# Kernel tuning notes

Hardware: AMD Instinct MI355X
Metric: run time of the kernel (lower is better)

## Reference

```python
import jax, jax.numpy as jnp
import numpy as np

NMS_PRE, NMS_POST, NMS_THRESH = 1024, 512, 0.7
B, A, FEAT = 4, 70400, 27648
BN_EPS = 1e-5


def _bev_iou(boxes):
    # boxes: [K, 7] (x, y, z, dx, dy, dz, ry); axis-aligned BEV IoU
    x, y, dx, dy = boxes[:, 0], boxes[:, 1], boxes[:, 3], boxes[:, 4]
    x1, x2 = x - 0.5 * dx, x + 0.5 * dx
    y1, y2 = y - 0.5 * dy, y + 0.5 * dy
    iw = jnp.clip(jnp.minimum(x2[:, None], x2[None, :]) - jnp.maximum(x1[:, None], x1[None, :]), 0.0)
    ih = jnp.clip(jnp.minimum(y2[:, None], y2[None, :]) - jnp.maximum(y1[:, None], y1[None, :]), 0.0)
    inter = iw * ih
    area = dx * dy
    return inter / jnp.clip(area[:, None] + area[None, :] - inter, 1e-6)


def _greedy_nms(boxes, thresh):
    # boxes sorted by score desc; returns keep mask [K]
    K = boxes.shape[0]
    iou = _bev_iou(boxes)
    idx = jnp.arange(K)

    def step(keep, i):
        sup = (iou[i] > thresh) & (idx > i) & keep[i]
        return keep & ~sup, None

    keep, _ = jax.lax.scan(step, jnp.ones(K, dtype=bool), jnp.arange(K))
    return keep


def _proposal_one(box, cls):
    # box: [A, 7], cls: [A, n_cls]  ->  padded rois [NPOST,7], scores [NPOST], labels [NPOST]
    score = jnp.max(cls, axis=-1)
    label = jnp.argmax(cls, axis=-1)
    top_score, top_idx = jax.lax.top_k(score, NMS_PRE)
    top_box = box[top_idx]
    keep = _greedy_nms(top_box, NMS_THRESH)
    # stable: kept entries first, preserving score order
    order = jnp.argsort(jnp.where(keep, jnp.arange(NMS_PRE), NMS_PRE + jnp.arange(NMS_PRE)))
    sel = order[:NMS_POST]
    valid = jnp.arange(NMS_POST) < jnp.minimum(jnp.sum(keep), NMS_POST)
    rois = jnp.where(valid[:, None], top_box[sel], 0.0)
    roi_score = jnp.where(valid, top_score[sel], 0.0)
    roi_label = jnp.where(valid, label[top_idx][sel], 0) + 1  # +1 as in module
    return rois, roi_score, roi_label


def _bn_relu(h, g, b):
    # eval-mode BN with running_mean=0, running_var=1
    return jax.nn.relu(h * (g / jnp.sqrt(1.0 + BN_EPS)) + b)


def _decode(reg, anchors):
    # ResidualCoder_v1.decode_torch
    xa, ya, za = anchors[..., 0], anchors[..., 1], anchors[..., 2]
    dxa, dya, dza, ra = anchors[..., 3], anchors[..., 4], anchors[..., 5], anchors[..., 6]
    xt, yt, zt = reg[..., 0], reg[..., 1], reg[..., 2]
    dxt, dyt, dzt, rt = reg[..., 3], reg[..., 4], reg[..., 5], reg[..., 6]
    diag = jnp.sqrt(dxa * dxa + dya * dya)
    return jnp.stack([
        xt * diag + xa, yt * diag + ya, zt * dza + za,
        jnp.exp(dxt) * dxa, jnp.exp(dyt) * dya, jnp.exp(dzt) * dza,
        rt + ra], axis=-1)


def _rotate_z(box, ang):
    # rotate x,y of box [..., 7] by ang [...]
    c, s = jnp.cos(ang), jnp.sin(ang)
    x = box[..., 0] * c - box[..., 1] * s
    y = box[..., 0] * s + box[..., 1] * c
    return jnp.concatenate([x[..., None], y[..., None], box[..., 2:]], axis=-1)


def reference(rpn_box_preds, rpn_cls_preds, pooled_features,
              Ws1, g1, b1, Ws2, g2, b2,
              Wc1, gc1, bc1, Wc2, gc2, bc2, Wc3, bc3,
              Wr1, gr1, br1, Wr2, gr2, br2, Wr3, br3):
    # proposal_layer: per-batch topk + NMS + padded scatter (vmapped)
    rois, roi_scores, roi_labels = jax.vmap(_proposal_one)(rpn_box_preds, rpn_cls_preds)

    # shared / cls / reg heads (1x1 Conv1d == per-roi MLP), dropout off (eval)
    x = _bn_relu(pooled_features @ Ws1.T, g1, b1)
    x = _bn_relu(x @ Ws2.T, g2, b2)
    c = _bn_relu(x @ Wc1.T, gc1, bc1)
    c = _bn_relu(c @ Wc2.T, gc2, bc2)
    cls_preds = c @ Wc3.T + bc3          # [B*NPOST, 1]
    r = _bn_relu(x @ Wr1.T, gr1, br1)
    r = _bn_relu(r @ Wr2.T, gr2, br2)
    reg_preds = r @ Wr3.T + br3          # [B*NPOST, 7]

    bsz = rois.shape[0]
    cls_preds = cls_preds.reshape(bsz, -1, cls_preds.shape[-1])
    reg_preds = reg_preds.reshape(bsz, -1, 7)

    # generate_predict_box: decode against detached rois with xyz zeroed
    anchors = jax.lax.stop_gradient(rois)
    anchors = anchors.at[..., 0:3].set(0.0)
    box_ct = _decode(reg_preds, anchors)
    box_preds = _rotate_z(box_ct, rois[..., 6])
    box_preds = jnp.concatenate([box_preds[..., 0:3] + rois[..., 0:3], box_preds[..., 3:]], axis=-1)

    return jnp.concatenate([cls_preds, box_preds, roi_scores[..., None]], axis=-1)  # [B, NPOST, 9]


def setup_inputs():
    key = jax.random.key(0)
    ks = jax.random.split(key, 32)
    u = jax.random.uniform(ks[0], (B, A, 7), dtype=jnp.float32)
    lo = jnp.array([0.0, -40.0, -2.0, 1.5, 1.4, 1.0, -3.14159], jnp.float32)
    hi = jnp.array([70.0, 40.0, 0.0, 4.5, 2.0, 2.0, 3.14159], jnp.float32)
    rpn_box_preds = lo + u * (hi - lo)
    rpn_cls_preds = jax.random.normal(ks[1], (B, A, 3), dtype=jnp.float32)
    pooled_features = jax.random.normal(ks[2], (B * NMS_POST, FEAT), dtype=jnp.float32) * 0.1

    def w(k, o, i, std=None):
        s = (1.0 / np.sqrt(i)) if std is None else std
        return jax.random.normal(k, (o, i), dtype=jnp.float32) * s

    d = dict(
        rpn_box_preds=rpn_box_preds, rpn_cls_preds=rpn_cls_preds, pooled_features=pooled_features,
        Ws1=w(ks[3], 256, FEAT), g1=jnp.ones(256), b1=jnp.zeros(256),
        Ws2=w(ks[4], 256, 256), g2=jnp.ones(256), b2=jnp.zeros(256),
        Wc1=w(ks[5], 256, 256), gc1=jnp.ones(256), bc1=jnp.zeros(256),
        Wc2=w(ks[6], 256, 256), gc2=jnp.ones(256), bc2=jnp.zeros(256),
        Wc3=w(ks[7], 1, 256), bc3=jnp.zeros(1),
        Wr1=w(ks[8], 256, 256), gr1=jnp.ones(256), br1=jnp.zeros(256),
        Wr2=w(ks[9], 256, 256), gr2=jnp.ones(256), br2=jnp.zeros(256),
        Wr3=w(ks[10], 7, 256, std=0.001), br3=jnp.zeros(7),
    )
    return d
```

## Files before the change

### kernel.cpp

```cpp
#include <hip/hip_runtime.h>
#include <cstdint>

typedef unsigned int u32;
typedef unsigned long long u64;
typedef unsigned short u16;

#define BATCH 4
#define A_CNT 70400
#define FEAT 27648
#define KSPLIT 16
#define KCHUNK 1728
#define NTILE_IT 27

typedef __attribute__((ext_vector_type(8))) short bf16x8;
typedef __attribute__((ext_vector_type(4))) float f32x4;
typedef __attribute__((ext_vector_type(4))) u32 u32x4;

constexpr size_t OF_KEYS = 0;
constexpr size_t OF_TBOX = OF_KEYS + 1126400;
constexpr size_t OF_TSC  = OF_TBOX + 114688;
constexpr size_t OF_BX1  = OF_TSC + 16384;
constexpr size_t OF_BX2  = OF_BX1 + 16384;
constexpr size_t OF_BY1  = OF_BX2 + 16384;
constexpr size_t OF_BY2  = OF_BY1 + 16384;
constexpr size_t OF_BAR  = OF_BY2 + 16384;
constexpr size_t OF_MASK = OF_BAR + 16384;
constexpr size_t OF_ROIS = OF_MASK + 524288;
constexpr size_t OF_RSC  = OF_ROIS + 57344;
constexpr size_t OF_BSW  = OF_RSC + 8192;
constexpr size_t OF_PART = OF_BSW + 14155776;
constexpr size_t WS_NEED = OF_PART + 33554432;

__device__ __forceinline__ u32 keyOf(float f) {
  u32 u = __float_as_uint(f);
  return (u & 0x80000000u) ? ~u : (u | 0x80000000u);
}
__device__ __forceinline__ float keyToF(u32 k) {
  u32 u = (k & 0x80000000u) ? (k ^ 0x80000000u) : ~k;
  return __uint_as_float(u);
}
__device__ __forceinline__ u16 f2bf(float f) {
  u32 u = __float_as_uint(f);
  u32 r = 0x7FFFu + ((u >> 16) & 1u);
  return (u16)((u + r) >> 16);
}
__device__ __forceinline__ void gload_lds16(const void* g, void* l) {
  auto gp = reinterpret_cast<const __attribute__((address_space(1))) unsigned int*>(
      reinterpret_cast<uintptr_t>(g));
  auto lp = reinterpret_cast<__attribute__((address_space(3))) unsigned int*>(
      reinterpret_cast<uintptr_t>(l));
  __builtin_amdgcn_global_load_lds(gp, lp, 16, 0, 0);
}
__device__ __forceinline__ u64 shflx64(u64 v, int m) {
  u32 lo = (u32)v, hi = (u32)(v >> 32);
  lo = __shfl_xor(lo, m, 64);
  hi = __shfl_xor(hi, m, 64);
  return ((u64)hi << 32) | lo;
}

__global__ __launch_bounds__(1024) void k_fatA(const float* __restrict__ cls,
    const float* __restrict__ Ws1, u32* __restrict__ keys, u32* __restrict__ Bsw)
{
  int bid = blockIdx.x;
  int t = threadIdx.x;
  if (bid < 864) {
    u32 w = (u32)bid * 1024u + t;
    u32 tile = w >> 11;
    u32 rem = w & 2047u;
    u32 n = rem >> 3;
    u32 pq = (rem & 7u) << 4;
    u32 q0 = pq ^ ((n & 7u) << 4);
    u32 col0 = tile * 64u + (q0 >> 1);
    const float* src = Ws1 + (size_t)n * FEAT + col0;
    float4 f0 = *(const float4*)src;
    float4 f1 = *(const float4*)(src + 4);
    u32x4 o;
    o.x = (u32)f2bf(f0.x) | ((u32)f2bf(f0.y) << 16);
    o.y = (u32)f2bf(f0.z) | ((u32)f2bf(f0.w) << 16);
    o.z = (u32)f2bf(f1.x) | ((u32)f2bf(f1.y) << 16);
    o.w = (u32)f2bf(f1.z) | ((u32)f2bf(f1.w) << 16);
    ((u32x4*)Bsw)[w] = o;
    return;
  }
  u32 g = (u32)(bid - 864) * 1024u + t;
  float s0 = cls[(size_t)g * 3 + 0];
  float s1 = cls[(size_t)g * 3 + 1];
  float s2 = cls[(size_t)g * 3 + 2];
  keys[g] = keyOf(fmaxf(s0, fmaxf(s1, s2)));
}

__global__ __launch_bounds__(1024) void k_prop(const u32* __restrict__ keys,
    const float* __restrict__ boxes, float* __restrict__ tbox, float* __restrict__ tsc,
    float* __restrict__ bx1, float* __restrict__ bx2, float* __restrict__ by1,
    float* __restrict__ by2, float* __restrict__ bar)
{
  int b = blockIdx.x, t = threadIdx.x;
  int lane = t & 63, wv = t >> 6;
  const u32* kb = keys + (size_t)b * A_CNT;
  __shared__ u64 s[2048];
  __shared__ u32 partials[16];
  __shared__ u32 cc;
  u32 h[35];
#pragma unroll
  for (int j = 0; j < 35; ++j) {
    int g0 = t + ((2 * j) << 10);
    int g1 = t + ((2 * j + 1) << 10);
    u32 a = (g0 < A_CNT) ? (kb[g0] >> 16) : 0u;
    u32 c2 = (g1 < A_CNT) ? (kb[g1] >> 16) : 0u;
    h[j] = a | (c2 << 16);
  }
  if (t == 0) cc = 0u;
  u32 lo = 0, hi = 65536;
  while (hi - lo > 1) {
    u32 mid = (lo + hi) >> 1;
    u32 c = 0;
#pragma unroll
    for (int j = 0; j < 35; ++j) {
      c += ((h[j] & 0xFFFFu) >= mid) ? 1u : 0u;
      c += ((h[j] >> 16) >= mid) ? 1u : 0u;
    }
#pragma unroll
    for (int o = 32; o > 0; o >>= 1) c += __shfl_xor(c, o, 64);
    __syncthreads();
    if (lane == 0) partials[wv] = c;
    __syncthreads();
    u32 tot = 0;
#pragma unroll
    for (int w2 = 0; w2 < 16; ++w2) tot += partials[w2];
    if (tot >= 1024u) lo = mid; else hi = mid;
  }
  u32 kth = lo;
  __syncthreads();
  u32 kc = kb[t];
#pragma unroll 1
  for (int i = 0; i < 69; ++i) {
    int g = t + (i << 10);
    u32 k = kc;
    if (i < 68) {
      int gn = t + ((i + 1) << 10);
      kc = (gn < A_CNT) ? kb[gn] : 0u;
    }
    bool pass = (g < A_CNT) && ((k >> 16) >= kth);
    u64 mm = __ballot(pass);
    if (mm) {
      int leader = __ffsll((unsigned long long)mm) - 1;
      u32 base = 0;
      if (lane == leader) base = atomicAdd(&cc, (u32)__popcll(mm));
      base = __shfl(base, leader, 64);
      if (pass) {
        u32 pos = base + (u32)__popcll(mm & ((1ull << lane) - 1ull));
        if (pos < 2048u) s[pos] = ((u64)k << 32) | (u32)(~(u32)g);
      }
    }
  }
  __syncthreads();
  u32 m = cc; if (m > 2048u) m = 2048u;
  for (int e = t; e < 2048; e += 1024) if (e >= (int)m) s[e] = 0ull;
  __syncthreads();
  {
    u64 v0 = s[2 * t], v1 = s[2 * t + 1];
#pragma unroll
    for (u32 k = 2; k <= 128; k <<= 1) {
      bool desc = ((t & (k >> 1)) == 0);
#pragma unroll
      for (u32 j = (k >> 1); j >= 2; j >>= 1) {
        u32 mmk = j >> 1;
        u64 p0 = shflx64(v0, mmk);
        u64 p1 = shflx64(v1, mmk);
        bool up = ((t & mmk) == 0);
        bool mx = (desc == up);
        v0 = mx ? (v0 > p0 ? v0 : p0) : (v0 < p0 ? v0 : p0);
        v1 = mx ? (v1 > p1 ? v1 : p1) : (v1 < p1 ? v1 : p1);
      }
      if (desc ? (v0 < v1) : (v0 > v1)) { u64 tmp = v0; v0 = v1; v1 = tmp; }
    }
    s[2 * t] = v0; s[2 * t + 1] = v1;
    __syncthreads();
    for (u32 k = 256; k <= 2048; k <<= 1) {
      for (u32 j = k >> 1; j >= 128; j >>= 1) {
        for (int e = t; e < 2048; e += 1024) {
          u32 p = (u32)e ^ j;
          if (p > (u32)e) {
            bool d2 = ((e & k) == 0);
            u64 x = s[e], y = s[p];
            if (d2 ? (x < y) : (x > y)) { s[e] = y; s[p] = x; }
          }
        }
        __syncthreads();
      }
      u64 v0 = s[2 * t], v1 = s[2 * t + 1];
      bool desc = ((t & (k >> 1)) == 0);
#pragma unroll
      for (u32 j = 64; j >= 2; j >>= 1) {
        u32 mmk = j >> 1;
        u64 p0 = shflx64(v0, mmk);
        u64 p1 = shflx64(v1, mmk);
        bool up = ((t & mmk) == 0);
        bool mx = (desc == up);
        v0 = mx ? (v0 > p0 ? v0 : p0) : (v0 < p0 ? v0 : p0);
        v1 = mx ? (v1 > p1 ? v1 : p1) : (v1 < p1 ? v1 : p1);
      }
      if (desc ? (v0 < v1) : (v0 > v1)) { u64 tmp = v0; v0 = v1; v1 = tmp; }
      s[2 * t] = v0; s[2 * t + 1] = v1;
      __syncthreads();
    }
  }
  u64 comp = s[t];
  u32 kk = (u32)(comp >> 32);
  u32 a = ~(u32)(comp & 0xFFFFFFFFull);
  int o = b * 1024 + t;
  tsc[o] = keyToF(kk);
  const float* bp = boxes + ((size_t)b * A_CNT + a) * 7;
  float x = bp[0], y = bp[1], z = bp[2], dx = bp[3], dy = bp[4], dz = bp[5], rr = bp[6];
  float* tb = tbox + (size_t)o * 7;
  tb[0] = x; tb[1] = y; tb[2] = z; tb[3] = dx; tb[4] = dy; tb[5] = dz; tb[6] = rr;
  {
#pragma clang fp contract(off)
    bx1[o] = x - 0.5f * dx; bx2[o] = x + 0.5f * dx;
    by1[o] = y - 0.5f * dy; by2[o] = y + 0.5f * dy;
    bar[o] = dx * dy;
  }
}

__global__ __launch_bounds__(256) void k_fatB(const float* __restrict__ A,
    const u32* __restrict__ Bsw, float* __restrict__ part,
    const float* __restrict__ bx1, const float* __restrict__ bx2,
    const float* __restrict__ by1, const float* __restrict__ by2,
    const float* __restrict__ bar, u32* __restrict__ mask)
{
  __shared__ __align__(16) char smem[73728];
  int bid = blockIdx.x;
  if (bid >= 512) {
    int mi = bid - 512;
    int b = mi >> 6;
    int cbk = (mi >> 2) & 15;
    int rb0 = (mi & 3) * 4;
    int tt = threadIdx.x;
    int rbi = tt >> 6, ln = tt & 63;
    int r = (rb0 + rbi) * 64 + ln;
    int o = b * 1024, jc0 = cbk * 64;
    float* cx1 = (float*)(smem);
    float* cx2 = (float*)(smem + 256);
    float* cy1 = (float*)(smem + 512);
    float* cy2 = (float*)(smem + 768);
    float* car = (float*)(smem + 1024);
    if (tt < 64) {
      cx1[tt] = bx1[o + jc0 + tt]; cx2[tt] = bx2[o + jc0 + tt];
      cy1[tt] = by1[o + jc0 + tt]; cy2[tt] = by2[o + jc0 + tt];
      car[tt] = bar[o + jc0 + tt];
    }
    __syncthreads();
    float rx1 = bx1[o + r], rx2 = bx2[o + r], ry1 = by1[o + r], ry2 = by2[o + r], rar = bar[o + r];
    u32 w0 = 0, w1 = 0;
    {
#pragma clang fp contract(off)
      for (int c = 0; c < 64; ++c) {
        int jc = jc0 + c;
        float iw = fminf(rx2, cx2[c]) - fmaxf(rx1, cx1[c]); iw = fmaxf(iw, 0.0f);
        float ih = fminf(ry2, cy2[c]) - fmaxf(ry1, cy1[c]); ih = fmaxf(ih, 0.0f);
        float inter = iw * ih;
        float den = fmaxf(rar + car[c] - inter, 1e-6f);
        float iou = inter / den;
        if ((iou > 0.7f) && (jc > r)) {
          if (c < 32) w0 |= 1u << c; else w1 |= 1u << (c - 32);
        }
      }
    }
    mask[((size_t)(o + r)) * 32 + cbk * 2 + 0] = w0;
    mask[((size_t)(o + r)) * 32 + cbk * 2 + 1] = w1;
    return;
  }
  int q = bid >> 3;
  int ks = (bid & 7) * 2 + (q >> 5);
  int mt = q & 31;
  int tid = threadIdx.x, lane = tid & 63, wv = tid >> 6;

  f32x4 acc[4][4];
#pragma unroll
  for (int i = 0; i < 4; ++i)
#pragma unroll
    for (int j = 0; j < 4; ++j) acc[i][j] = (f32x4){0.f, 0.f, 0.f, 0.f};

  int am = tid >> 2;
  int ak = (tid & 3) * 16;
  const float* ap_base = A + ((size_t)(mt * 64 + am)) * FEAT + (size_t)ks * KCHUNK + ak;
  int asw = (am & 7) << 4;
  int ac0 = (tid & 3) * 32;
  int awoff0 = am * 128 + (ac0 ^ asw);
  int awoff1 = am * 128 + ((ac0 + 16) ^ asw);
  const char* bsrc_base = (const char*)Bsw + ((size_t)(ks * NTILE_IT)) * 32768 + (wv * 8) * 1024 + lane * 16;
  int bdoff = (wv * 8) * 1024;

  int row16 = lane & 15, kgrp = lane >> 4;
  int aoff[4][2], boff[4][2];
#pragma unroll
  for (int ksub = 0; ksub < 2; ++ksub) {
    int qq = ksub * 64 + kgrp * 16;
#pragma unroll
    for (int mf = 0; mf < 4; ++mf) {
      int row = mf * 16 + row16;
      aoff[mf][ksub] = row * 128 + (qq ^ ((row & 7) << 4));
    }
#pragma unroll
    for (int nf = 0; nf < 4; ++nf) {
      int n = wv * 64 + nf * 16 + row16;
      boff[nf][ksub] = n * 128 + (qq ^ ((n & 7) << 4));
    }
  }

  char* Albuf = smem;
  {
    const float4* ap = (const float4*)ap_base;
    float4 f0 = ap[0], f1 = ap[1], f2 = ap[2], f3 = ap[3];
    u32x4 c0, c1;
    c0.x = (u32)f2bf(f0.x) | ((u32)f2bf(f0.y) << 16);
    c0.y = (u32)f2bf(f0.z) | ((u32)f2bf(f0.w) << 16);
    c0.z = (u32)f2bf(f1.x) | ((u32)f2bf(f1.y) << 16);
    c0.w = (u32)f2bf(f1.z) | ((u32)f2bf(f1.w) << 16);
    c1.x = (u32)f2bf(f2.x) | ((u32)f2bf(f2.y) << 16);
    c1.y = (u32)f2bf(f2.z) | ((u32)f2bf(f2.w) << 16);
    c1.z = (u32)f2bf(f3.x) | ((u32)f2bf(f3.y) << 16);
    c1.w = (u32)f2bf(f3.z) | ((u32)f2bf(f3.w) << 16);
    *(u32x4*)(Albuf + awoff0) = c0;
    *(u32x4*)(Albuf + awoff1) = c1;
#pragma unroll
    for (int i = 0; i < 8; ++i)
      gload_lds16(bsrc_base + i * 1024, smem + 8192 + bdoff + i * 1024);
  }
  __syncthreads();

  for (int it = 0; it < NTILE_IT; ++it) {
    char* Bcur = smem + 8192 + ((it & 1) ? 32768 : 0);
    char* Bnxt = smem + 8192 + ((it & 1) ? 0 : 32768);
    bool has = (it + 1 < NTILE_IT);
    float4 f0n, f1n, f2n, f3n;
    if (has) {
      const float4* ap = (const float4*)(ap_base + (it + 1) * 64);
      f0n = ap[0]; f1n = ap[1]; f2n = ap[2]; f3n = ap[3];
    }
    bf16x8 af[4][2], bfv[4][2];
#pragma unroll
    for (int ksub = 0; ksub < 2; ++ksub) {
#pragma unroll
      for (int mf = 0; mf < 4; ++mf) af[mf][ksub] = *(const bf16x8*)(Albuf + aoff[mf][ksub]);
#pragma unroll
      for (int nf = 0; nf < 4; ++nf) bfv[nf][ksub] = *(const bf16x8*)(Bcur + boff[nf][ksub]);
    }
    __syncthreads();
    if (has) {
      u32x4 c0, c1;
      c0.x = (u32)f2bf(f0n.x) | ((u32)f2bf(f0n.y) << 16);
      c0.y = (u32)f2bf(f0n.z) | ((u32)f2bf(f0n.w) << 16);
      c0.z = (u32)f2bf(f1n.x) | ((u32)f2bf(f1n.y) << 16);
      c0.w = (u32)f2bf(f1n.z) | ((u32)f2bf(f1n.w) << 16);
      c1.x = (u32)f2bf(f2n.x) | ((u32)f2bf(f2n.y) << 16);
      c1.y = (u32)f2bf(f2n.z) | ((u32)f2bf(f2n.w) << 16);
      c1.z = (u32)f2bf(f3n.x) | ((u32)f2bf(f3n.y) << 16);
      c1.w = (u32)f2bf(f3n.z) | ((u32)f2bf(f3n.w) << 16);
      *(u32x4*)(Albuf + awoff0) = c0;
      *(u32x4*)(Albuf + awoff1) = c1;
      const char* bs = bsrc_base + (size_t)(it + 1) * 32768;
#pragma unroll
      for (int i = 0; i < 8; ++i)
        gload_lds16(bs + i * 1024, Bnxt + bdoff + i * 1024);
    }
#pragma unroll
    for (int ksub = 0; ksub < 2; ++ksub)
#pragma unroll
      for (int mf = 0; mf < 4; ++mf)
#pragma unroll
        for (int nf = 0; nf < 4; ++nf)
          acc[mf][nf] = __builtin_amdgcn_mfma_f32_16x16x32_bf16(af[mf][ksub], bfv[nf][ksub], acc[mf][nf], 0, 0, 0);
    __syncthreads();
  }
  float* pb = part + (size_t)ks * 524288;
#pragma unroll
  for (int mf = 0; mf < 4; ++mf) {
    int row = mt * 64 + mf * 16 + kgrp * 4;
#pragma unroll
    for (int nf = 0; nf < 4; ++nf) {
      int col = wv * 64 + nf * 16 + row16;
#pragma unroll
      for (int rr = 0; rr < 4; ++rr)
        pb[(size_t)(row + rr) * 256 + col] = acc[mf][nf][rr];
    }
  }
}

__global__ __launch_bounds__(64) void k_nms(const u32* __restrict__ mask,
    const float* __restrict__ tbox, const float* __restrict__ tsc,
    float* __restrict__ rois, float* __restrict__ rsc)
{
  int b = blockIdx.x;
  int lane = threadIdx.x;
  int el = lane & 31;
  const u32* M = mask + (size_t)b * 1024 * 32;
  u32 R = 0;
  u32 cur[32], nxt[32];
#pragma unroll
  for (int i = 0; i < 32; ++i) cur[i] = M[(size_t)(i * 32 + el)];
#pragma unroll 1
  for (int c = 0; c < 32; ++c) {
    if (c < 31) {
      int nb = (c + 1) * 1024 + el;
#pragma unroll
      for (int i = 0; i < 32; ++i) nxt[i] = M[(size_t)(nb + i * 32)];
    }
    u32 w = R;
#pragma unroll
    for (int i = 0; i < 32; ++i) w |= ((w >> i) & 1u) ? 0u : cur[i];
    u32 wfin = __shfl(w, c, 64);
#pragma unroll
    for (int i = 0; i < 32; ++i) R |= ((wfin >> i) & 1u) ? 0u : cur[i];
#pragma unroll
    for (int i = 0; i < 32; ++i) cur[i] = nxt[i];
  }
  u32 keepw = (lane < 32) ? ~R : 0u;
  int c = __popc(keepw);
  int pre = c;
  for (int d = 1; d < 64; d <<= 1) {
    int v = __shfl_up(pre, d, 64);
    if (lane >= d) pre += v;
  }
  int total = __shfl(pre, 31, 64);
  int base = pre - c;
  if (lane < 32) {
    u32 w = keepw;
    int rank = base;
    while (w) {
      int bit = __ffs(w) - 1;
      w &= w - 1;
      if (rank < 512) {
        int r = lane * 32 + bit;
        const float* tb = tbox + ((size_t)b * 1024 + r) * 7;
        float* rp = rois + ((size_t)b * 512 + rank) * 7;
        rp[0] = tb[0]; rp[1] = tb[1]; rp[2] = tb[2]; rp[3] = tb[3];
        rp[4] = tb[4]; rp[5] = tb[5]; rp[6] = tb[6];
        rsc[b * 512 + rank] = tsc[b * 1024 + r];
      }
      rank++;
    }
  }
  for (int z = total + lane; z < 512; z += 64) {
    float* rp = rois + ((size_t)b * 512 + z) * 7;
    rp[0] = rp[1] = rp[2] = rp[3] = rp[4] = rp[5] = rp[6] = 0.0f;
    rsc[b * 512 + z] = 0.0f;
  }
}

__device__ __forceinline__ void layer4(const float (*IN)[256], const float* __restrict__ W,
    const float* __restrict__ g, const float* __restrict__ bb, float (*OUT)[256], int t, int h)
{
  float acc[4] = {0, 0, 0, 0};
  const float* Wrow = W + (size_t)t * 256;
  for (int k = 0; k < 256; k += 4) {
    float4 w4 = *(const float4*)&Wrow[k];
#pragma unroll
    for (int r = 0; r < 4; ++r) {
      float4 xv = *(const float4*)&IN[h * 4 + r][k];
      acc[r] = fmaf(xv.x, w4.x, acc[r]);
      acc[r] = fmaf(xv.y, w4.y, acc[r]);
      acc[r] = fmaf(xv.z, w4.z, acc[r]);
      acc[r] = fmaf(xv.w, w4.w, acc[r]);
    }
  }
  float sc = g[t] / sqrtf(1.0f + 1e-5f);
  float bv = bb[t];
#pragma unroll
  for (int r = 0; r < 4; ++r)
    OUT[h * 4 + r][t] = fmaxf(fmaf(acc[r], sc, bv), 0.0f);
}

__global__ __launch_bounds__(512) void k_chain(const float* __restrict__ part,
    const float* __restrict__ Ws2, const float* __restrict__ Wc1, const float* __restrict__ Wc2,
    const float* __restrict__ Wr1, const float* __restrict__ Wr2,
    const float* __restrict__ g1, const float* __restrict__ b1,
    const float* __restrict__ g2, const float* __restrict__ b2,
    const float* __restrict__ gc1, const float* __restrict__ bc1,
    const float* __restrict__ gc2, const float* __restrict__ bc2,
    const float* __restrict__ gr1, const float* __restrict__ br1,
    const float* __restrict__ gr2, const float* __restrict__ br2,
    const float* __restrict__ Wc3, const float* __restrict__ bc3,
    const float* __restrict__ Wr3, const float* __restrict__ br3,
    const float* __restrict__ rois, const float* __restrict__ rsc,
    float* __restrict__ out)
{
  int bid = blockIdx.x, tid = threadIdx.x;
  int t = tid & 255, h = tid >> 8;
  __shared__ __align__(16) float bufX[8][256];
  __shared__ __align__(16) float bufY[8][256];
  __shared__ __align__(16) float bufC[8][256];
  __shared__ __align__(16) float bufR[8][256];
  __shared__ float hd[64];
  {
    float sc = g1[t] / sqrtf(1.0f + 1e-5f);
    float bv = b1[t];
#pragma unroll
    for (int r = 0; r < 4; ++r) {
      int row = h * 4 + r;
      float s = 0.f;
#pragma unroll
      for (int ks = 0; ks < KSPLIT; ++ks)
        s += part[(size_t)ks * 524288 + (size_t)(bid * 8 + row) * 256 + t];
      bufX[row][t] = fmaxf(fmaf(s, sc, bv), 0.0f);
    }
  }
  __syncthreads();
  layer4(bufX, Ws2, g2, b2, bufY, t, h);
  __syncthreads();
  layer4(bufY, Wc1, gc1, bc1, bufC, t, h);
  layer4(bufY, Wr1, gr1, br1, bufR, t, h);
  __syncthreads();
  layer4(bufC, Wc2, gc2, bc2, bufX, t, h);
  layer4(bufR, Wr2, gr2, br2, bufY, t, h);
  __syncthreads();
  int wv = tid >> 6, ln = tid & 63;
  for (int task = wv; task < 64; task += 8) {
    float p;
    if (task < 8) {
      float4 yv = *(const float4*)&bufX[task][ln * 4];
      float4 w4 = ((const float4*)Wc3)[ln];
      p = yv.x * w4.x + yv.y * w4.y + yv.z * w4.z + yv.w * w4.w;
    } else {
      int i = task - 8, row = i / 7, j = i % 7;
      float4 yv = *(const float4*)&bufY[row][ln * 4];
      float4 w4 = ((const float4*)(Wr3 + j * 256))[ln];
      p = yv.x * w4.x + yv.y * w4.y + yv.z * w4.z + yv.w * w4.w;
    }
#pragma unroll
    for (int off = 32; off > 0; off >>= 1) p += __shfl_xor(p, off, 64);
    if (ln == 0) hd[task] = p;
  }
  __syncthreads();
  if (tid < 8) {
    int m = bid * 8 + tid;
    float clsv = hd[tid] + bc3[0];
    float rg[7];
#pragma unroll
    for (int j = 0; j < 7; ++j) rg[j] = hd[8 + tid * 7 + j] + br3[j];
    const float* R = rois + (size_t)m * 7;
    float rx = R[0], ry = R[1], rz = R[2], dxa = R[3], dya = R[4], dza = R[5], ra = R[6];
    float diag = sqrtf(dxa * dxa + dya * dya);
    float x = rg[0] * diag, y = rg[1] * diag, z = rg[2] * dza;
    float ex = expf(rg[3]) * dxa, ey = expf(rg[4]) * dya, ez = expf(rg[5]) * dza;
    float hr = rg[6] + ra;
    float cc = cosf(ra), sn = sinf(ra);
    float xr = x * cc - y * sn, yr = x * sn + y * cc;
    float* O = out + (size_t)m * 9;
    O[0] = clsv; O[1] = xr + rx; O[2] = yr + ry; O[3] = z + rz;
    O[4] = ex; O[5] = ey; O[6] = ez; O[7] = hr; O[8] = rsc[m];
  }
}

extern "C" void kernel_launch(void* const* d_in, const int* in_sizes, int n_in,
                              void* d_out, int out_size, void* d_ws, size_t ws_size,
                              hipStream_t stream)
{
  const float* rpn_box = (const float*)d_in[0];
  const float* rpn_cls = (const float*)d_in[1];
  const float* pooled  = (const float*)d_in[2];
  const float* Ws1 = (const float*)d_in[3];
  const float* g1  = (const float*)d_in[4];
  const float* b1  = (const float*)d_in[5];
  const float* Ws2 = (const float*)d_in[6];
  const float* g2  = (const float*)d_in[7];
  const float* b2  = (const float*)d_in[8];
  const float* Wc1 = (const float*)d_in[9];
  const float* gc1 = (const float*)d_in[10];
  const float* bc1 = (const float*)d_in[11];
  const float* Wc2 = (const float*)d_in[12];
  const float* gc2 = (const float*)d_in[13];
  const float* bc2 = (const float*)d_in[14];
  const float* Wc3 = (const float*)d_in[15];
  const float* bc3 = (const float*)d_in[16];
  const float* Wr1 = (const float*)d_in[17];
  const float* gr1 = (const float*)d_in[18];
  const float* br1 = (const float*)d_in[19];
  const float* Wr2 = (const float*)d_in[20];
  const float* gr2 = (const float*)d_in[21];
  const float* br2 = (const float*)d_in[22];
  const float* Wr3 = (const float*)d_in[23];
  const float* br3 = (const float*)d_in[24];

  if (ws_size < WS_NEED) return;

  char* ws = (char*)d_ws;
  u32* keys = (u32*)(ws + OF_KEYS);
  float* tbox = (float*)(ws + OF_TBOX);
  float* tsc  = (float*)(ws + OF_TSC);
  float* bx1 = (float*)(ws + OF_BX1);
  float* bx2 = (float*)(ws + OF_BX2);
  float* by1 = (float*)(ws + OF_BY1);
  float* by2 = (float*)(ws + OF_BY2);
  float* bar = (float*)(ws + OF_BAR);
  u32* mask = (u32*)(ws + OF_MASK);
  float* roisb = (float*)(ws + OF_ROIS);
  float* rscb  = (float*)(ws + OF_RSC);
  u32* Bsw = (u32*)(ws + OF_BSW);
  float* part = (float*)(ws + OF_PART);

  k_fatA<<<1139, 1024, 0, stream>>>(rpn_cls, Ws1, keys, Bsw);
  k_prop<<<4, 1024, 0, stream>>>(keys, rpn_box, tbox, tsc, bx1, bx2, by1, by2, bar);
  k_fatB<<<768, 256, 0, stream>>>(pooled, Bsw, part, bx1, bx2, by1, by2, bar, mask);
  k_nms<<<4, 64, 0, stream>>>(mask, tbox, tsc, roisb, rscb);
  k_chain<<<256, 512, 0, stream>>>(part, Ws2, Wc1, Wc2, Wr1, Wr2,
                                   g1, b1, g2, b2, gc1, bc1, gc2, bc2,
                                   gr1, br1, gr2, br2, Wc3, bc3, Wr3, br3,
                                   roisb, rscb, (float*)d_out);
}
```

Before: 265.8 us.

## Enlarge GEMM M-tile to 128 rows and move double buffering from B to A

The split-K GEMM block now computes a 128x256 output tile instead of 64x256, halving the number of GEMM blocks and the number of times each bf16 weight tile is fetched. The A operand (fp32 converted to bf16) is now double-buffered in LDS, while B is single-buffered and refilled right after its fragments are read into registers. A packing helper replaces the repeated conversion code. The cost is twice as many accumulator registers per thread and only 256 GEMM blocks, which may reduce occupancy and latency hiding on the streaming A loads.

```diff
diff --git a/kernel.cpp b/kernel.cpp
--- a/kernel.cpp
+++ b/kernel.cpp
@@ -56,6 +56,14 @@
   lo = __shfl_xor(lo, m, 64);
   hi = __shfl_xor(hi, m, 64);
   return ((u64)hi << 32) | lo;
+}
+__device__ __forceinline__ u32x4 pack8(float4 a, float4 b) {
+  u32x4 o;
+  o.x = (u32)f2bf(a.x) | ((u32)f2bf(a.y) << 16);
+  o.y = (u32)f2bf(a.z) | ((u32)f2bf(a.w) << 16);
+  o.z = (u32)f2bf(b.x) | ((u32)f2bf(b.y) << 16);
+  o.w = (u32)f2bf(b.z) | ((u32)f2bf(b.w) << 16);
+  return o;
 }
 
 __global__ __launch_bounds__(1024) void k_fatA(const float* __restrict__ cls,
@@ -74,12 +82,7 @@
     const float* src = Ws1 + (size_t)n * FEAT + col0;
     float4 f0 = *(const float4*)src;
     float4 f1 = *(const float4*)(src + 4);
-    u32x4 o;
-    o.x = (u32)f2bf(f0.x) | ((u32)f2bf(f0.y) << 16);
-    o.y = (u32)f2bf(f0.z) | ((u32)f2bf(f0.w) << 16);
-    o.z = (u32)f2bf(f1.x) | ((u32)f2bf(f1.y) << 16);
-    o.w = (u32)f2bf(f1.z) | ((u32)f2bf(f1.w) << 16);
-    ((u32x4*)Bsw)[w] = o;
+    ((u32x4*)Bsw)[w] = pack8(f0, f1);
     return;
   }
   u32 g = (u32)(bid - 864) * 1024u + t;
@@ -228,10 +231,10 @@
     const float* __restrict__ by1, const float* __restrict__ by2,
     const float* __restrict__ bar, u32* __restrict__ mask)
 {
-  __shared__ __align__(16) char smem[73728];
+  __shared__ __align__(16) char smem[65536];
   int bid = blockIdx.x;
-  if (bid >= 512) {
-    int mi = bid - 512;
+  if (bid >= 256) {
+    int mi = bid - 256;
     int b = mi >> 6;
     int cbk = (mi >> 2) & 15;
     int rb0 = (mi & 3) * 4;
@@ -270,34 +273,35 @@
     mask[((size_t)(o + r)) * 32 + cbk * 2 + 1] = w1;
     return;
   }
-  int q = bid >> 3;
-  int ks = (bid & 7) * 2 + (q >> 5);
-  int mt = q & 31;
+  int ks = bid & 15;
+  int mt = bid >> 4;
   int tid = threadIdx.x, lane = tid & 63, wv = tid >> 6;
 
-  f32x4 acc[4][4];
-#pragma unroll
-  for (int i = 0; i < 4; ++i)
+  f32x4 acc[8][4];
+#pragma unroll
+  for (int i = 0; i < 8; ++i)
 #pragma unroll
     for (int j = 0; j < 4; ++j) acc[i][j] = (f32x4){0.f, 0.f, 0.f, 0.f};
 
-  int am = tid >> 2;
-  int ak = (tid & 3) * 16;
-  const float* ap_base = A + ((size_t)(mt * 64 + am)) * FEAT + (size_t)ks * KCHUNK + ak;
+  int am = tid >> 1;
+  int ak = (tid & 1) * 32;
+  const float* ap_base = A + ((size_t)(mt * 128 + am)) * FEAT + (size_t)ks * KCHUNK + ak;
   int asw = (am & 7) << 4;
-  int ac0 = (tid & 3) * 32;
-  int awoff0 = am * 128 + (ac0 ^ asw);
-  int awoff1 = am * 128 + ((ac0 + 16) ^ asw);
+  int aw0 = am * 128 + (((tid & 1) * 64 +  0) ^ asw);
+  int aw1 = am * 128 + (((tid & 1) * 64 + 16) ^ asw);
+  int aw2 = am * 128 + (((tid & 1) * 64 + 32) ^ asw);
+  int aw3 = am * 128 + (((tid & 1) * 64 + 48) ^ asw);
   const char* bsrc_base = (const char*)Bsw + ((size_t)(ks * NTILE_IT)) * 32768 + (wv * 8) * 1024 + lane * 16;
   int bdoff = (wv * 8) * 1024;
+  char* Bbuf = smem + 32768;
 
   int row16 = lane & 15, kgrp = lane >> 4;
-  int aoff[4][2], boff[4][2];
+  int aoff[8][2], boff[4][2];
 #pragma unroll
   for (int ksub = 0; ksub < 2; ++ksub) {
     int qq = ksub * 64 + kgrp * 16;
 #pragma unroll
-    for (int mf = 0; mf < 4; ++mf) {
+    for (int mf = 0; mf < 8; ++mf) {
       int row = mf * 16 + row16;
       aoff[mf][ksub] = row * 128 + (qq ^ ((row & 7) << 4));
     }
@@ -308,75 +312,64 @@
     }
   }
 
-  char* Albuf = smem;
   {
     const float4* ap = (const float4*)ap_base;
-    float4 f0 = ap[0], f1 = ap[1], f2 = ap[2], f3 = ap[3];
-    u32x4 c0, c1;
-    c0.x = (u32)f2bf(f0.x) | ((u32)f2bf(f0.y) << 16);
-    c0.y = (u32)f2bf(f0.z) | ((u32)f2bf(f0.w) << 16);
-    c0.z = (u32)f2bf(f1.x) | ((u32)f2bf(f1.y) << 16);
-    c0.w = (u32)f2bf(f1.z) | ((u32)f2bf(f1.w) << 16);
-    c1.x = (u32)f2bf(f2.x) | ((u32)f2bf(f2.y) << 16);
-    c1.y = (u32)f2bf(f2.z) | ((u32)f2bf(f2.w) << 16);
-    c1.z = (u32)f2bf(f3.x) | ((u32)f2bf(f3.y) << 16);
-    c1.w = (u32)f2bf(f3.z) | ((u32)f2bf(f3.w) << 16);
-    *(u32x4*)(Albuf + awoff0) = c0;
-    *(u32x4*)(Albuf + awoff1) = c1;
+    float4 g0 = ap[0], g1 = ap[1], g2 = ap[2], g3 = ap[3];
+    float4 g4 = ap[4], g5 = ap[5], g6 = ap[6], g7 = ap[7];
+    *(u32x4*)(smem + aw0) = pack8(g0, g1);
+    *(u32x4*)(smem + aw1) = pack8(g2, g3);
+    *(u32x4*)(smem + aw2) = pack8(g4, g5);
+    *(u32x4*)(smem + aw3) = pack8(g6, g7);
 #pragma unroll
     for (int i = 0; i < 8; ++i)
-      gload_lds16(bsrc_base + i * 1024, smem + 8192 + bdoff + i * 1024);
+      gload_lds16(bsrc_base + i * 1024, Bbuf + bdoff + i * 1024);
   }
   __syncthreads();
 
   for (int it = 0; it < NTILE_IT; ++it) {
-    char* Bcur = smem + 8192 + ((it & 1) ? 32768 : 0);
-    char* Bnxt = smem + 8192 + ((it & 1) ? 0 : 32768);
+    char* Acur = smem + ((it & 1) ? 16384 : 0);
+    char* Anxt = smem + ((it & 1) ? 0 : 16384);
     bool has = (it + 1 < NTILE_IT);
-    float4 f0n, f1n, f2n, f3n;
+    float4 g0, g1, g2, g3, g4, g5, g6, g7;
     if (has) {
       const float4* ap = (const float4*)(ap_base + (it + 1) * 64);
-      f0n = ap[0]; f1n = ap[1]; f2n = ap[2]; f3n = ap[3];
-    }
-    bf16x8 af[4][2], bfv[4][2];
-#pragma unroll
-    for (int ksub = 0; ksub < 2; ++ksub) {
-#pragma unroll
-      for (int mf = 0; mf < 4; ++mf) af[mf][ksub] = *(const bf16x8*)(Albuf + aoff[mf][ksub]);
-#pragma unroll
-      for (int nf = 0; nf < 4; ++nf) bfv[nf][ksub] = *(const bf16x8*)(Bcur + boff[nf][ksub]);
-    }
+      g0 = ap[0]; g1 = ap[1]; g2 = ap[2]; g3 = ap[3];
+      g4 = ap[4]; g5 = ap[5]; g6 = ap[6]; g7 = ap[7];
+    }
+    bf16x8 bfv[4][2];
+#pragma unroll
+    for (int ksub = 0; ksub < 2; ++ksub)
+#pragma unroll
+      for (int nf = 0; nf < 4; ++nf)
+        bfv[nf][ksub] = *(const bf16x8*)(Bbuf + boff[nf][ksub]);
     __syncthreads();
     if (has) {
-      u32x4 c0, c1;
-      c0.x = (u32)f2bf(f0n.x) | ((u32)f2bf(f0n.y) << 16);
-      c0.y = (u32)f2bf(f0n.z) | ((u32)f2bf(f0n.w) << 16);
-      c0.z = (u32)f2bf(f1n.x) | ((u32)f2bf(f1n.y) << 16);
-      c0.w = (u32)f2bf(f1n.z) | ((u32)f2bf(f1n.w) << 16);
-      c1.x = (u32)f2bf(f2n.x) | ((u32)f2bf(f2n.y) << 16);
-      c1.y = (u32)f2bf(f2n.z) | ((u32)f2bf(f2n.w) << 16);
-      c1.z = (u32)f2bf(f3n.x) | ((u32)f2bf(f3n.y) << 16);
-      c1.w = (u32)f2bf(f3n.z) | ((u32)f2bf(f3n.w) << 16);
-      *(u32x4*)(Albuf + awoff0) = c0;
-      *(u32x4*)(Albuf + awoff1) = c1;
       const char* bs = bsrc_base + (size_t)(it + 1) * 32768;
 #pragma unroll
       for (int i = 0; i < 8; ++i)
-        gload_lds16(bs + i * 1024, Bnxt + bdoff + i * 1024);
+        gload_lds16(bs + i * 1024, Bbuf + bdoff + i * 1024);
     }
 #pragma unroll
     for (int ksub = 0; ksub < 2; ++ksub)
 #pragma unroll
-      for (int mf = 0; mf < 4; ++mf)
+      for (int mf = 0; mf < 8; ++mf) {
+        bf16x8 af = *(const bf16x8*)(Acur + aoff[mf][ksub]);
 #pragma unroll
         for (int nf = 0; nf < 4; ++nf)
-          acc[mf][nf] = __builtin_amdgcn_mfma_f32_16x16x32_bf16(af[mf][ksub], bfv[nf][ksub], acc[mf][nf], 0, 0, 0);
+          acc[mf][nf] = __builtin_amdgcn_mfma_f32_16x16x32_bf16(af, bfv[nf][ksub], acc[mf][nf], 0, 0, 0);
+      }
+    if (has) {
+      *(u32x4*)(Anxt + aw0) = pack8(g0, g1);
+      *(u32x4*)(Anxt + aw1) = pack8(g2, g3);
+      *(u32x4*)(Anxt + aw2) = pack8(g4, g5);
+      *(u32x4*)(Anxt + aw3) = pack8(g6, g7);
+    }
     __syncthreads();
   }
   float* pb = part + (size_t)ks * 524288;
 #pragma unroll
-  for (int mf = 0; mf < 4; ++mf) {
-    int row = mt * 64 + mf * 16 + kgrp * 4;
+  for (int mf = 0; mf < 8; ++mf) {
+    int row = mt * 128 + mf * 16 + kgrp * 4;
 #pragma unroll
     for (int nf = 0; nf < 4; ++nf) {
       int col = wv * 64 + nf * 16 + row16;
@@ -601,7 +594,7 @@
 
   k_fatA<<<1139, 1024, 0, stream>>>(rpn_cls, Ws1, keys, Bsw);
   k_prop<<<4, 1024, 0, stream>>>(keys, rpn_box, tbox, tsc, bx1, bx2, by1, by2, bar);
-  k_fatB<<<768, 256, 0, stream>>>(pooled, Bsw, part, bx1, bx2, by1, by2, bar, mask);
+  k_fatB<<<512, 256, 0, stream>>>(pooled, Bsw, part, bx1, bx2, by1, by2, bar, mask);
   k_nms<<<4, 64, 0, stream>>>(mask, tbox, tsc, roisb, rscb);
   k_chain<<<256, 512, 0, stream>>>(part, Ws2, Wc1, Wc2, Wr1, Wr2,
                                    g1, b1, g2, b2, gc1, bc1, gc2, bc2,
```

After: 275.9 us. 1.04x slower.
